# Kernel tuning notes

Hardware: AMD Instinct MI355X
Metric: run time of the kernel (lower is better)

The kernel has to match this reference:

```python
import jax, jax.numpy as jnp
import numpy as np

N = 50000
E = 800000
F = 128


def gcn_smooth(edge_index, x):
    """Symmetric-normalized GCN smoothing: D^-1/2 (A + I) D^-1/2 x.

    edge_index: [2, E] int (src, dst) of a sparse graph; self-loops added here.
    x: [N, F] float node features.
    """
    src, dst = edge_index[0], edge_index[1]
    n = x.shape[0]
    # degree of A + I
    deg = jax.ops.segment_sum(jnp.ones((src.shape[0],), x.dtype), dst, num_segments=n) + 1.0
    dinv = jax.lax.rsqrt(deg)  # [N]
    # per-edge normalization d^-1/2[src] * d^-1/2[dst]
    norm_e = dinv[src] * dinv[dst]  # [E]
    msg = x[src] * norm_e[:, None]  # [E, F] -- gather + scale
    agg = jax.ops.segment_sum(msg, dst, num_segments=n)  # scatter-add over dst
    # self-loop contribution: dinv[i]^2 * x[i]
    return agg + (dinv * dinv)[:, None] * x


def setup_inputs() -> dict:
    key = jax.random.key(0)
    ks = jax.random.split(key, 12)
    inp = {
        "X_HypGNet": jax.random.normal(ks[0], (N, F), jnp.float32),
        "X_CGNet": jax.random.normal(ks[1], (N, F), jnp.float32),
        "X_SGNet": jax.random.normal(ks[2], (N, F), jnp.float32),
        "edge_index_hyp": jax.random.randint(ks[3], (2, E), 0, N, dtype=jnp.int32),
        "edge_index_c": jax.random.randint(ks[4], (2, E), 0, N, dtype=jnp.int32),
        "edge_index_s": jax.random.randint(ks[5], (2, E), 0, N, dtype=jnp.int32),
        "W_hyp": jax.random.normal(ks[6], (F, F), jnp.float32) * 0.05,
        "b_hyp": jax.random.normal(ks[7], (F,), jnp.float32) * 0.05,
        "W_cg": jax.random.normal(ks[8], (F, F), jnp.float32) * 0.05,
        "b_cg": jax.random.normal(ks[9], (F,), jnp.float32) * 0.05,
        "W_sg": jax.random.normal(ks[10], (F, F), jnp.float32) * 0.05,
        "b_sg": jax.random.normal(ks[11], (F,), jnp.float32) * 0.05,
    }
    return inp


def reference(X_HypGNet, X_CGNet, X_SGNet, edge_index_hyp, edge_index_c, edge_index_s,
              W_hyp, b_hyp, W_cg, b_cg, W_sg, b_sg):
    X_hyp = X_HypGNet @ W_hyp + b_hyp
    X_cg = X_CGNet @ W_cg + b_cg
    X_sg = X_SGNet @ W_sg + b_sg
    X_hyp_s = gcn_smooth(edge_index_hyp, X_hyp)
    X_cg_s = gcn_smooth(edge_index_c, X_cg)
    X_sg_s = gcn_smooth(edge_index_s, X_sg)
    return (X_hyp_s, X_cg_s, X_sg_s)
```

## Files before the change

kernel.cpp:

```cpp
#include <hip/hip_runtime.h>

#define F_DIM 128
#define NG 3
#define AEPT 16
#define CAP 48
#define MAXBIN 256
#define SPILL_CAP 8192

typedef __attribute__((ext_vector_type(8))) short short8_t;
typedef __attribute__((ext_vector_type(4))) float f32x4;

__device__ __forceinline__ unsigned short f2bf(float f) {
    unsigned int x = __float_as_uint(f);
    unsigned int r = x + 0x7fffu + ((x >> 16) & 1u);
    return (unsigned short)(r >> 16);
}
__device__ __forceinline__ float bflo(unsigned int u) { return __uint_as_float(u << 16); }
__device__ __forceinline__ float bfhi(unsigned int u) { return __uint_as_float(u & 0xffff0000u); }

struct GArgs {
    const int* src[NG]; const int* dst[NG];
    const float* X[NG]; const float* W[NG]; const float* b[NG];
    float* out[NG];
    unsigned short* Xps[NG];
    unsigned short* sorted[NG];
    int* binbuf[NG];
    int* bincur[NG];
    int* cstore[NG];
    float* dinv[NG];
    int* spill[NG];
    int* spill_n[NG];
    int nbin, bincap;
};

__global__ __launch_bounds__(256) void init_kernel(GArgs a, int g0) {
    int g = g0 + blockIdx.y;
    for (int i = threadIdx.x; i < a.nbin; i += 256) a.bincur[g][i] = i * a.bincap;
    if (threadIdx.x == 0) a.spill_n[g][0] = 0;
}

__global__ __launch_bounds__(256) void binA_kernel(GArgs a, int g0, int E) {
    int g = g0 + blockIdx.y;
    __shared__ int cnt[MAXBIN];
    __shared__ int lcur[MAXBIN];
    const int t = threadIdx.x;
    const int nbin = a.nbin, bincap = a.bincap;
    for (int i = t; i < nbin; i += 256) cnt[i] = 0;
    __syncthreads();
    const int* dst = a.dst[g];
    const int* src = a.src[g];
    const int base = blockIdx.x * (256 * AEPT) + t;
    int dd[AEPT], sv[AEPT];
#pragma unroll
    for (int i = 0; i < AEPT; ++i) {
        int e = base + i * 256;
        int ec = (e < E) ? e : 0;
        dd[i] = __builtin_nontemporal_load(&dst[ec]);
        sv[i] = __builtin_nontemporal_load(&src[ec]);
        if (e < E) atomicAdd(&cnt[dd[i] >> 8], 1);
    }
    __syncthreads();
    for (int i = t; i < nbin; i += 256) {
        int c = cnt[i];
        lcur[i] = c ? atomicAdd(&a.bincur[g][i], c) : 0;
    }
    __syncthreads();
    int* binbuf = a.binbuf[g];
#pragma unroll
    for (int i = 0; i < AEPT; ++i) {
        int e = base + i * 256;
        if (e < E) {
            int bin = dd[i] >> 8;
            int pos = atomicAdd(&lcur[bin], 1);
            if (pos < (bin + 1) * bincap) {
                binbuf[pos] = ((dd[i] & 255) << 16) | sv[i];
            } else {
                int sp = atomicAdd(a.spill_n[g], 1);
                if (sp < SPILL_CAP) {
                    a.spill[g][2 * sp] = sv[i];
                    a.spill[g][2 * sp + 1] = dd[i];
                }
            }
        }
    }
}

__global__ __launch_bounds__(256) void binB_kernel(GArgs a, int g0, int n) {
    int g = g0 + blockIdx.y;
    int bin = blockIdx.x;
    const int t = threadIdx.x;
    __shared__ int cnt[256];
    cnt[t] = 0;
    __syncthreads();
    const int bincap = a.bincap;
    int used = a.bincur[g][bin] - bin * bincap;
    int rd = min(used, bincap);
    const int* bb = a.binbuf[g] + bin * bincap;
    unsigned short* sorted = a.sorted[g];
    for (int j = t; j < rd; j += 256) {
        int u = bb[j];
        int dl = u >> 16;
        int s = u & 0xffff;
        int tk = atomicAdd(&cnt[dl], 1);
        int d = (bin << 8) + dl;
        if (tk < CAP) {
            sorted[d * CAP + tk] = (unsigned short)s;
        } else {
            int sp = atomicAdd(a.spill_n[g], 1);
            if (sp < SPILL_CAP) {
                a.spill[g][2 * sp] = s;
                a.spill[g][2 * sp + 1] = d;
            }
        }
    }
    __syncthreads();
    int d = (bin << 8) + t;
    if (d < n) {
        int deg = cnt[t];
        a.cstore[g][d] = min(deg, CAP);
        a.dinv[g][d] = rsqrtf((float)deg + 1.0f);
    }
}

__global__ __launch_bounds__(256) void gemm_kernel(GArgs a, int g0, int n) {
    int g = g0 + blockIdx.y;
    __shared__ unsigned short Xl[128 * 128];
    __shared__ unsigned short Wt[128 * 128];
    const int t = threadIdx.x;
    const int row0 = blockIdx.x * 128;
    const float* X = a.X[g];
    const float* W = a.W[g];
    char* XlB = (char*)Xl;
    char* WtB = (char*)Wt;

    for (int i = t; i < 128 * 16; i += 256) {
        int r = i >> 4, kc = i & 15;
        int row = row0 + r;
        float4 x0 = make_float4(0.f, 0.f, 0.f, 0.f), x1 = x0;
        if (row < n) {
            const float4* xp = (const float4*)(X + (size_t)row * F_DIM + kc * 8);
            x0 = xp[0]; x1 = xp[1];
        }
        uint4 pk;
        pk.x = (unsigned)f2bf(x0.x) | ((unsigned)f2bf(x0.y) << 16);
        pk.y = (unsigned)f2bf(x0.z) | ((unsigned)f2bf(x0.w) << 16);
        pk.z = (unsigned)f2bf(x1.x) | ((unsigned)f2bf(x1.y) << 16);
        pk.w = (unsigned)f2bf(x1.z) | ((unsigned)f2bf(x1.w) << 16);
        unsigned int ad = (unsigned)((r << 8) + (kc << 4)) ^ (unsigned)((r & 15) << 4);
        *(uint4*)(XlB + ad) = pk;
    }
    for (int i = t; i < 128 * 16; i += 256) {
        int nn = i & 127, kc = i >> 7;
        const float* wp = W + (size_t)(kc * 8) * F_DIM + nn;
        uint4 pk;
        pk.x = (unsigned)f2bf(wp[0])   | ((unsigned)f2bf(wp[128]) << 16);
        pk.y = (unsigned)f2bf(wp[256]) | ((unsigned)f2bf(wp[384]) << 16);
        pk.z = (unsigned)f2bf(wp[512]) | ((unsigned)f2bf(wp[640]) << 16);
        pk.w = (unsigned)f2bf(wp[768]) | ((unsigned)f2bf(wp[896]) << 16);
        unsigned int ad = (unsigned)((nn << 8) + (kc << 4)) ^ (unsigned)((nn & 15) << 4);
        *(uint4*)(WtB + ad) = pk;
    }
    __syncthreads();

    const int l = t & 63;
    const int wv = t >> 6;
    const int wr = wv >> 1, wc = wv & 1;
    const int lm = l & 15;
    const int lk = l >> 4;

    f32x4 acc[4][4] = {};
#pragma unroll
    for (int ks = 0; ks < 4; ++ks) {
        const int kb = ks * 64 + lk * 16;
        short8_t af[4], bv[4];
#pragma unroll
        for (int mt = 0; mt < 4; ++mt) {
            int r = wr * 64 + mt * 16 + lm;
            unsigned int ad = (unsigned)((r << 8) + kb) ^ (unsigned)((r & 15) << 4);
            af[mt] = *(const short8_t*)(XlB + ad);
        }
#pragma unroll
        for (int nt = 0; nt < 4; ++nt) {
            int c = wc * 64 + nt * 16 + lm;
            unsigned int ad = (unsigned)((c << 8) + kb) ^ (unsigned)((c & 15) << 4);
            bv[nt] = *(const short8_t*)(WtB + ad);
        }
#pragma unroll
        for (int mt = 0; mt < 4; ++mt)
#pragma unroll
            for (int nt = 0; nt < 4; ++nt)
                acc[mt][nt] = __builtin_amdgcn_mfma_f32_16x16x32_bf16(af[mt], bv[nt],
                                                                      acc[mt][nt], 0, 0, 0);
    }

    const float* bia = a.b[g];
    const float* dinv = a.dinv[g];
    unsigned short* Xps = a.Xps[g];
#pragma unroll
    for (int nt = 0; nt < 4; ++nt) {
        int col = wc * 64 + nt * 16 + lm;
        float bc = bia[col];
#pragma unroll
        for (int mt = 0; mt < 4; ++mt) {
            int rbase = row0 + wr * 64 + mt * 16 + lk * 4;
#pragma unroll
            for (int r = 0; r < 4; ++r) {
                int row = rbase + r;
                if (row < n) {
                    float v = (acc[mt][nt][r] + bc) * dinv[row];
                    Xps[(size_t)row * F_DIM + col] = f2bf(v);
                }
            }
        }
    }
}

__global__ __launch_bounds__(256) void agg_kernel(GArgs a, int g0, int n) {
    int g = g0 + blockIdx.y;
    int wave = (blockIdx.x * 256 + threadIdx.x) >> 6;
    if (wave >= n) return;
    int lane = threadIdx.x & 63;
    const unsigned int* Xp = (const unsigned int*)a.Xps[g];
    const unsigned short* sorted = a.sorted[g];
    int beg = wave * CAP;
    int cnt = a.cstore[g][wave];
    unsigned int u0 = Xp[(size_t)wave * 64 + lane];
    float ax = bflo(u0), ay = bfhi(u0);
    for (int j = 0; j < cnt;) {
        int m = min(cnt - j, 64);
        int s = (j + lane < cnt)
                    ? (int)__builtin_nontemporal_load(&sorted[beg + j + lane]) : 0;
        int k = 0;
        for (; k + 8 <= m; k += 8) {
            int s0 = __shfl(s, k + 0, 64), s1 = __shfl(s, k + 1, 64);
            int s2 = __shfl(s, k + 2, 64), s3 = __shfl(s, k + 3, 64);
            int s4 = __shfl(s, k + 4, 64), s5 = __shfl(s, k + 5, 64);
            int s6 = __shfl(s, k + 6, 64), s7 = __shfl(s, k + 7, 64);
            unsigned int v0 = Xp[(size_t)s0 * 64 + lane];
            unsigned int v1 = Xp[(size_t)s1 * 64 + lane];
            unsigned int v2 = Xp[(size_t)s2 * 64 + lane];
            unsigned int v3 = Xp[(size_t)s3 * 64 + lane];
            unsigned int v4 = Xp[(size_t)s4 * 64 + lane];
            unsigned int v5 = Xp[(size_t)s5 * 64 + lane];
            unsigned int v6 = Xp[(size_t)s6 * 64 + lane];
            unsigned int v7 = Xp[(size_t)s7 * 64 + lane];
            ax += bflo(v0); ay += bfhi(v0);
            ax += bflo(v1); ay += bfhi(v1);
            ax += bflo(v2); ay += bfhi(v2);
            ax += bflo(v3); ay += bfhi(v3);
            ax += bflo(v4); ay += bfhi(v4);
            ax += bflo(v5); ay += bfhi(v5);
            ax += bflo(v6); ay += bfhi(v6);
            ax += bflo(v7); ay += bfhi(v7);
        }
        if (k + 4 <= m) {
            int s0 = __shfl(s, k + 0, 64), s1 = __shfl(s, k + 1, 64);
            int s2 = __shfl(s, k + 2, 64), s3 = __shfl(s, k + 3, 64);
            unsigned int v0 = Xp[(size_t)s0 * 64 + lane];
            unsigned int v1 = Xp[(size_t)s1 * 64 + lane];
            unsigned int v2 = Xp[(size_t)s2 * 64 + lane];
            unsigned int v3 = Xp[(size_t)s3 * 64 + lane];
            ax += bflo(v0); ay += bfhi(v0);
            ax += bflo(v1); ay += bfhi(v1);
            ax += bflo(v2); ay += bfhi(v2);
            ax += bflo(v3); ay += bfhi(v3);
            k += 4;
        }
        for (; k < m; ++k) {
            int sk = __shfl(s, k, 64);
            unsigned int v = Xp[(size_t)sk * 64 + lane];
            ax += bflo(v);
            ay += bfhi(v);
        }
        j += m;
    }
    float dd = a.dinv[g][wave];
    ((float2*)a.out[g])[(size_t)wave * 64 + lane] = make_float2(ax * dd, ay * dd);
}

__global__ __launch_bounds__(128) void spill_kernel(GArgs a, int g0) {
    int g = g0 + blockIdx.y;
    int ns = min(a.spill_n[g][0], SPILL_CAP);
    const unsigned short* Xps = a.Xps[g];
    const float* dinv = a.dinv[g];
    float* out = a.out[g];
    for (int i = blockIdx.x; i < ns; i += gridDim.x) {
        int s = a.spill[g][2 * i];
        int d = a.spill[g][2 * i + 1];
        float w = dinv[d];
        int f = threadIdx.x;
        float v = __uint_as_float(((unsigned int)Xps[(size_t)s * F_DIM + f]) << 16);
        unsafeAtomicAdd(&out[(size_t)d * F_DIM + f], w * v);
    }
}

extern "C" void kernel_launch(void* const* d_in, const int* in_sizes, int n_in,
                              void* d_out, int out_size, void* d_ws, size_t ws_size,
                              hipStream_t stream) {
    const float* Xin[NG] = {(const float*)d_in[0], (const float*)d_in[1], (const float*)d_in[2]};
    const int* ei[NG] = {(const int*)d_in[3], (const int*)d_in[4], (const int*)d_in[5]};
    const float* Wk[NG] = {(const float*)d_in[6], (const float*)d_in[8], (const float*)d_in[10]};
    const float* bk[NG] = {(const float*)d_in[7], (const float*)d_in[9], (const float*)d_in[11]};

    const int N = in_sizes[0] / F_DIM;
    const int E = in_sizes[3] / 2;
    float* out = (float*)d_out;

    const int nbin = (N + 255) >> 8;
    const int bincap = E / nbin + E / (3 * nbin) + 256;

    const size_t xps_b = (size_t)N * F_DIM * 2;
    const size_t sorted_b = (size_t)N * CAP * 2;
    const size_t binbuf_b = (size_t)nbin * bincap * 4;
    const size_t nb = (size_t)N * 4;
    const size_t bincur_b = ((size_t)nbin * 4 + 255) / 256 * 256;
    const size_t spill_b = (size_t)SPILL_CAP * 8 + 64;
    const size_t per = ((xps_b + sorted_b + binbuf_b + 2 * nb + bincur_b + spill_b + 255)
                        / 256) * 256;
    const bool fused = ws_size >= (size_t)NG * per;
    char* base = (char*)d_ws;

    GArgs a;
    a.nbin = nbin;
    a.bincap = bincap;
    for (int r = 0; r < NG; ++r) {
        char* s = base + (size_t)(fused ? r : 0) * per;
        size_t off = 0;
        a.Xps[r] = (unsigned short*)(s + off); off += xps_b;
        a.sorted[r] = (unsigned short*)(s + off); off += sorted_b;
        a.binbuf[r] = (int*)(s + off); off += binbuf_b;
        a.cstore[r] = (int*)(s + off); off += nb;
        a.dinv[r] = (float*)(s + off); off += nb;
        a.bincur[r] = (int*)(s + off); off += bincur_b;
        a.spill[r] = (int*)(s + off);
        a.spill_n[r] = (int*)(s + off + spill_b - 64);
        a.src[r] = ei[r];
        a.dst[r] = ei[r] + E;
        a.X[r] = Xin[r];
        a.W[r] = Wk[r];
        a.b[r] = bk[r];
        a.out[r] = out + (size_t)r * N * F_DIM;
    }

    const dim3 blk(256);
    const int gAe = (E + 256 * AEPT - 1) / (256 * AEPT);
    const int gR = (N + 127) / 128;
    const int gG = (N * 64 + 255) / 256;

    if (fused) {
        init_kernel<<<dim3(1, NG), blk, 0, stream>>>(a, 0);
        binA_kernel<<<dim3(gAe, NG), blk, 0, stream>>>(a, 0, E);
        binB_kernel<<<dim3(nbin, NG), blk, 0, stream>>>(a, 0, N);
        gemm_kernel<<<dim3(gR, NG), blk, 0, stream>>>(a, 0, N);
        agg_kernel<<<dim3(gG, NG), blk, 0, stream>>>(a, 0, N);
        spill_kernel<<<dim3(16, NG), dim3(128), 0, stream>>>(a, 0);
    } else {
        for (int g = 0; g < NG; ++g) {
            init_kernel<<<dim3(1, 1), blk, 0, stream>>>(a, g);
            binA_kernel<<<dim3(gAe, 1), blk, 0, stream>>>(a, g, E);
            binB_kernel<<<dim3(nbin, 1), blk, 0, stream>>>(a, g, N);
            gemm_kernel<<<dim3(gR, 1), blk, 0, stream>>>(a, g, N);
            agg_kernel<<<dim3(gG, 1), blk, 0, stream>>>(a, g, N);
            spill_kernel<<<dim3(16, 1), dim3(128), 0, stream>>>(a, g);
        }
    }
}
```

Before: 194.8 us.

## Gather neighbor rows with 16-byte loads across four edge groups per wave

The aggregation kernel now splits each wave into four 16-lane groups. Each group loads a whole 256-byte bf16 row with uint4 loads, so a wave handles four edges per load step, two steps per loop iteration. Partial sums are combined with xor shuffles, and only the first group writes the output with float4 stores. The fused path now launches agg once per graph instead of one 3D grid. The goal is fewer, wider memory instructions in place of 4-byte per-lane gathers, at the cost of the cross-group reduction and idle lanes when a node's edge count is not a multiple of eight.

Result: slower. 201.6 us (+3.5%).

```diff
diff --git a/kernel.cpp b/kernel.cpp
--- a/kernel.cpp
+++ b/kernel.cpp
@@ -215,67 +215,53 @@
     }
 }
 
-__global__ __launch_bounds__(256) void agg_kernel(GArgs a, int g0, int n) {
-    int g = g0 + blockIdx.y;
+__global__ __launch_bounds__(256) void agg_kernel(GArgs a, int g, int n) {
     int wave = (blockIdx.x * 256 + threadIdx.x) >> 6;
     if (wave >= n) return;
-    int lane = threadIdx.x & 63;
-    const unsigned int* Xp = (const unsigned int*)a.Xps[g];
+    const int l = threadIdx.x & 63;
+    const int c = l & 15;
+    const int hi = l >> 4;
+    const uint4* Xp4 = (const uint4*)a.Xps[g];
     const unsigned short* sorted = a.sorted[g];
-    int beg = wave * CAP;
     int cnt = a.cstore[g][wave];
-    unsigned int u0 = Xp[(size_t)wave * 64 + lane];
-    float ax = bflo(u0), ay = bfhi(u0);
-    for (int j = 0; j < cnt;) {
-        int m = min(cnt - j, 64);
-        int s = (j + lane < cnt)
-                    ? (int)__builtin_nontemporal_load(&sorted[beg + j + lane]) : 0;
-        int k = 0;
-        for (; k + 8 <= m; k += 8) {
-            int s0 = __shfl(s, k + 0, 64), s1 = __shfl(s, k + 1, 64);
-            int s2 = __shfl(s, k + 2, 64), s3 = __shfl(s, k + 3, 64);
-            int s4 = __shfl(s, k + 4, 64), s5 = __shfl(s, k + 5, 64);
-            int s6 = __shfl(s, k + 6, 64), s7 = __shfl(s, k + 7, 64);
-            unsigned int v0 = Xp[(size_t)s0 * 64 + lane];
-            unsigned int v1 = Xp[(size_t)s1 * 64 + lane];
-            unsigned int v2 = Xp[(size_t)s2 * 64 + lane];
-            unsigned int v3 = Xp[(size_t)s3 * 64 + lane];
-            unsigned int v4 = Xp[(size_t)s4 * 64 + lane];
-            unsigned int v5 = Xp[(size_t)s5 * 64 + lane];
-            unsigned int v6 = Xp[(size_t)s6 * 64 + lane];
-            unsigned int v7 = Xp[(size_t)s7 * 64 + lane];
-            ax += bflo(v0); ay += bfhi(v0);
-            ax += bflo(v1); ay += bfhi(v1);
-            ax += bflo(v2); ay += bfhi(v2);
-            ax += bflo(v3); ay += bfhi(v3);
-            ax += bflo(v4); ay += bfhi(v4);
-            ax += bflo(v5); ay += bfhi(v5);
-            ax += bflo(v6); ay += bfhi(v6);
-            ax += bflo(v7); ay += bfhi(v7);
-        }
-        if (k + 4 <= m) {
-            int s0 = __shfl(s, k + 0, 64), s1 = __shfl(s, k + 1, 64);
-            int s2 = __shfl(s, k + 2, 64), s3 = __shfl(s, k + 3, 64);
-            unsigned int v0 = Xp[(size_t)s0 * 64 + lane];
-            unsigned int v1 = Xp[(size_t)s1 * 64 + lane];
-            unsigned int v2 = Xp[(size_t)s2 * 64 + lane];
-            unsigned int v3 = Xp[(size_t)s3 * 64 + lane];
-            ax += bflo(v0); ay += bfhi(v0);
-            ax += bflo(v1); ay += bfhi(v1);
-            ax += bflo(v2); ay += bfhi(v2);
-            ax += bflo(v3); ay += bfhi(v3);
-            k += 4;
-        }
-        for (; k < m; ++k) {
-            int sk = __shfl(s, k, 64);
-            unsigned int v = Xp[(size_t)sk * 64 + lane];
-            ax += bflo(v);
-            ay += bfhi(v);
-        }
-        j += m;
-    }
+    int s = (l < cnt) ? (int)__builtin_nontemporal_load(&sorted[(size_t)wave * CAP + l]) : 0;
+    float a0 = 0.f, a1 = 0.f, a2 = 0.f, a3 = 0.f, a4 = 0.f, a5 = 0.f, a6 = 0.f, a7 = 0.f;
+    for (int k = 0; k < cnt; k += 8) {
+        int e0 = k + hi, e1 = k + 4 + hi;
+        int s0 = __shfl(s, e0, 64);
+        int s1 = __shfl(s, e1 < 48 ? e1 : 0, 64);
+        uint4 v0 = Xp4[(size_t)s0 * 16 + c];
+        uint4 v1 = Xp4[(size_t)s1 * 16 + c];
+        if (e0 >= cnt) v0 = make_uint4(0u, 0u, 0u, 0u);
+        if (e1 >= cnt) v1 = make_uint4(0u, 0u, 0u, 0u);
+        a0 += bflo(v0.x); a1 += bfhi(v0.x);
+        a2 += bflo(v0.y); a3 += bfhi(v0.y);
+        a4 += bflo(v0.z); a5 += bfhi(v0.z);
+        a6 += bflo(v0.w); a7 += bfhi(v0.w);
+        a0 += bflo(v1.x); a1 += bfhi(v1.x);
+        a2 += bflo(v1.y); a3 += bfhi(v1.y);
+        a4 += bflo(v1.z); a5 += bfhi(v1.z);
+        a6 += bflo(v1.w); a7 += bfhi(v1.w);
+    }
+    a0 += __shfl_xor(a0, 16, 64); a0 += __shfl_xor(a0, 32, 64);
+    a1 += __shfl_xor(a1, 16, 64); a1 += __shfl_xor(a1, 32, 64);
+    a2 += __shfl_xor(a2, 16, 64); a2 += __shfl_xor(a2, 32, 64);
+    a3 += __shfl_xor(a3, 16, 64); a3 += __shfl_xor(a3, 32, 64);
+    a4 += __shfl_xor(a4, 16, 64); a4 += __shfl_xor(a4, 32, 64);
+    a5 += __shfl_xor(a5, 16, 64); a5 += __shfl_xor(a5, 32, 64);
+    a6 += __shfl_xor(a6, 16, 64); a6 += __shfl_xor(a6, 32, 64);
+    a7 += __shfl_xor(a7, 16, 64); a7 += __shfl_xor(a7, 32, 64);
+    uint4 v = Xp4[(size_t)wave * 16 + c];
+    a0 += bflo(v.x); a1 += bfhi(v.x);
+    a2 += bflo(v.y); a3 += bfhi(v.y);
+    a4 += bflo(v.z); a5 += bfhi(v.z);
+    a6 += bflo(v.w); a7 += bfhi(v.w);
     float dd = a.dinv[g][wave];
-    ((float2*)a.out[g])[(size_t)wave * 64 + lane] = make_float2(ax * dd, ay * dd);
+    if (hi == 0) {
+        float* o = (float*)a.out[g] + (size_t)wave * F_DIM + c * 8;
+        *(float4*)(o + 0) = make_float4(a0 * dd, a1 * dd, a2 * dd, a3 * dd);
+        *(float4*)(o + 4) = make_float4(a4 * dd, a5 * dd, a6 * dd, a7 * dd);
+    }
 }
 
 __global__ __launch_bounds__(128) void spill_kernel(GArgs a, int g0) {
@@ -352,7 +338,8 @@
         binA_kernel<<<dim3(gAe, NG), blk, 0, stream>>>(a, 0, E);
         binB_kernel<<<dim3(nbin, NG), blk, 0, stream>>>(a, 0, N);
         gemm_kernel<<<dim3(gR, NG), blk, 0, stream>>>(a, 0, N);
-        agg_kernel<<<dim3(gG, NG), blk, 0, stream>>>(a, 0, N);
+        for (int g = 0; g < NG; ++g)
+            agg_kernel<<<dim3(gG, 1), blk, 0, stream>>>(a, g, N);
         spill_kernel<<<dim3(16, NG), dim3(128), 0, stream>>>(a, 0);
     } else {
         for (int g = 0; g < NG; ++g) {
```
